# Performance work log

Measured on AMD Instinct MI355X. Metric: run time of the kernel, lower is better.

The kernel has to match this reference:

```python
import jax, jax.numpy as jnp
import numpy as np

D = 128       # embed_dim
UD = 128      # user_embed_dim
NU, NI, NR = 100000, 50000, 10
B, H, S = 4096, 50, 32
EPS = 1e-5


def setup_inputs() -> dict:
    key = jax.random.key(0)
    ks = jax.random.split(key, 24)
    p = lambda k, s: (jax.random.normal(k, s, jnp.float32) * 0.05)
    inp = {
        'u2e': p(ks[0], (NU, D)), 'v2e': p(ks[1], (NI, D)), 'r2e': p(ks[2], (NR, D)),
        'gv_w1': p(ks[3], (2 * D, D)), 'gv_b1': jnp.zeros(D),
        'gv_w2': p(ks[4], (D, D)), 'gv_b2': jnp.zeros(D),
        'atth_w1': p(ks[5], (2 * D, D)), 'atth_b1': jnp.zeros(D),
        'atth_w2': p(ks[6], (D, 1)), 'atth_b2': jnp.zeros(1),
        'enc_w': p(ks[7], (2 * D, D)), 'enc_b': jnp.zeros(D),
        'atts_w1': p(ks[8], (2 * D, D)), 'atts_b1': jnp.zeros(D),
        'atts_w2': p(ks[9], (D, 1)), 'atts_b2': jnp.zeros(1),
        'soc_w': p(ks[10], (2 * D, D)), 'soc_b': jnp.zeros(D),
        'attn_wa': p(ks[11], (D, D)), 'attn_ba': p(ks[12], (D,)),
        'fc1_w': p(ks[13], (D, D)), 'fc1_b': jnp.zeros(D),
        'bn1_g': jnp.ones(D), 'bn1_b': jnp.zeros(D),
        'fc2_w': p(ks[14], (D, UD)), 'fc2_b': jnp.zeros(UD),
        'efc1_w': p(ks[15], (2 * UD, D)), 'efc1_b': jnp.zeros(D),
        'bn2_g': jnp.ones(D), 'bn2_b': jnp.zeros(D),
        'efc2_w': p(ks[16], (D, UD)), 'efc2_b': jnp.zeros(UD),
        'user_ids': jax.random.randint(ks[17], (B, 2), 0, NU),
        'hist_items': jax.random.randint(ks[18], (2 * B, H), 0, NI),
        'hist_ratings': jax.random.randint(ks[19], (2 * B, H), 0, NR),
        'soc_neigh': jax.random.randint(ks[20], (2 * B, S), 0, NU),
    }
    return inp


def _forward(u2e, v2e, r2e, gv_w1, gv_b1, gv_w2, gv_b2, atth_w1, atth_b1, atth_w2, atth_b2,
             enc_w, enc_b, atts_w1, atts_b1, atts_w2, atts_b2, soc_w, soc_b, attn_wa, attn_ba,
             fc1_w, fc1_b, bn1_g, bn1_b, fc2_w, fc2_b, efc1_w, efc1_b, bn2_g, bn2_b,
             efc2_w, efc2_b, user_ids, hist_items, hist_ratings, soc_neigh):
    u = u2e[user_ids.reshape(-1)]                                   # [N,D]
    # --- UV_Aggregator: rating-history aggregation with attention ---
    x = jnp.concatenate([v2e[hist_items], r2e[hist_ratings]], -1)   # [N,H,2D]
    x = jax.nn.relu(x @ gv_w1 + gv_b1)
    x = jax.nn.relu(x @ gv_w2 + gv_b2)                              # [N,H,D]
    q = jnp.broadcast_to(u[:, None, :], x.shape)
    e = jax.nn.relu(jnp.concatenate([x, q], -1) @ atth_w1 + atth_b1) @ atth_w2 + atth_b2
    a = jax.nn.softmax(e, axis=1)                                   # [N,H,1]
    agg = jnp.sum(a * x, axis=1)                                    # [N,D]
    # --- UV_Encoder ---
    h_hist = jax.nn.relu(jnp.concatenate([u, agg], -1) @ enc_w + enc_b)
    # --- Social_Aggregator: neighbor aggregation with attention ---
    nf = u2e[soc_neigh]                                             # [N,S,D]
    qn = jnp.broadcast_to(u[:, None, :], nf.shape)
    es = jax.nn.relu(jnp.concatenate([nf, qn], -1) @ atts_w1 + atts_b1) @ atts_w2 + atts_b2
    a_s = jax.nn.softmax(es, axis=1)
    agg_s = jnp.sum(a_s * nf, axis=1)                               # [N,D]
    # --- Social_Encoder ---
    h = jax.nn.relu(jnp.concatenate([h_hist, agg_s], -1) @ soc_w + soc_b)
    hp = h.reshape(-1, 2, D)                                        # [B,2,D] (initiator, respondent)
    # --- SelfAttentionBatch over each pair ---
    ap = jax.nn.softmax(jnp.tanh(hp @ attn_wa) @ attn_ba, axis=1)   # [B,2]
    w = ap[..., None] * hp                                          # [B,2,D]
    # --- social project head: fc1 -> BN (per-pair batch of 2, train mode) -> relu -> fc2 ---
    y = w @ fc1_w + fc1_b                                           # [B,2,D]
    mu = y.mean(axis=1, keepdims=True)
    var = y.var(axis=1, keepdims=True)
    y = (y - mu) * jax.lax.rsqrt(var + EPS) * bn1_g + bn1_b
    y = jax.nn.relu(y) @ fc2_w + fc2_b                              # [B,2,UD]
    ini, res = y[:, 0], y[:, 1]
    # --- esocial head on concatenated pair reps: fc -> BN over batch -> relu -> fc ---
    c = y.reshape(y.shape[0], -1)                                   # [B,2*UD]
    z = c @ efc1_w + efc1_b                                         # [B,D]
    z = (z - z.mean(0)) * jax.lax.rsqrt(z.var(0) + EPS) * bn2_g + bn2_b
    z = jax.nn.relu(z) @ efc2_w + efc2_b                            # [B,UD]
    return z, ini, res


def reference(u2e, v2e, r2e, gv_w1, gv_b1, gv_w2, gv_b2, atth_w1, atth_b1, atth_w2, atth_b2,
              enc_w, enc_b, atts_w1, atts_b1, atts_w2, atts_b2, soc_w, soc_b, attn_wa, attn_ba,
              fc1_w, fc1_b, bn1_g, bn1_b, fc2_w, fc2_b, efc1_w, efc1_b, bn2_g, bn2_b,
              efc2_w, efc2_b, user_ids, hist_items, hist_ratings, soc_neigh):
    return _forward(u2e, v2e, r2e, gv_w1, gv_b1, gv_w2, gv_b2, atth_w1, atth_b1, atth_w2,
                    atth_b2, enc_w, enc_b, atts_w1, atts_b1, atts_w2, atts_b2, soc_w, soc_b,
                    attn_wa, attn_ba, fc1_w, fc1_b, bn1_g, bn1_b, fc2_w, fc2_b, efc1_w,
                    efc1_b, bn2_g, bn2_b, efc2_w, efc2_b, user_ids, hist_items,
                    hist_ratings, soc_neigh)
```

## Files before the change

kernel.cpp:

```cpp
#include <hip/hip_runtime.h>
#include <hip/hip_bf16.h>
#include <math.h>

#define NROWS   8192
#define HLEN    50
#define SLEN    32
#define NPAIR   4096

typedef __attribute__((ext_vector_type(8))) short   short8;
typedef __attribute__((ext_vector_type(8))) __bf16  b8;
typedef __attribute__((ext_vector_type(4))) float   f32x4;
typedef unsigned short us;

#define A_GV_B1    0
#define A_GV_B2    128
#define A_ATTH_B1  256
#define A_ATTH_W2  384
#define A_ENC_W    512
#define A_ENC_B    33280
#define A_ATTS_B1  33408
#define A_ATTS_W2  33536
#define A_SOC_W    33664
#define A_SOC_B    66432
#define A_ATTN_WA  66560
#define A_ATTN_BA  82944
#define A_FC1_W    83072
#define A_FC1_B    99456
#define A_BN1_G    99584
#define A_BN1_B    99712
#define A_FC2_W    99840
#define A_FC2_B    116224
#define A_EFC1_W   116352
#define A_EFC1_B   149120
#define A_BN2_G    149248
#define A_BN2_B    149376
#define A_EFC2_W   149504
#define A_EFC2_B   165888
#define A_TOTAL    166016

#define WS_HR    0u
#define WS_Z     2097152u
#define WS_ST    4194304u
#define WS_WP1   4195328u
#define WS_WP2   4260864u
#define WS_WPA   4293632u
#define WS_WPS   4359168u
#define WS_AR    4424704u
#define WS_UB    4757504u
#define WS_VB    30357504u
#define WS_RB    43157504u
#define WS2_NEED 43160064u

__device__ __forceinline__ float b2f(us u){
  unsigned int x = ((unsigned int)u) << 16; float f;
  __builtin_memcpy(&f, &x, 4); return f;
}
__device__ __forceinline__ us f2b(float f){
  unsigned int x; __builtin_memcpy(&x, &f, 4);
  return (us)((x + 0x7fffu + ((x >> 16) & 1u)) >> 16);
}
__device__ __forceinline__ us f2bc(float f){
  unsigned int x; __builtin_memcpy(&x, &f, 4);
  return (us)((x + 0x8000u) >> 16);
}
__device__ __forceinline__ float relu(float x){ return 0.5f * (x + fabsf(x)); }

__device__ __forceinline__ b8 f8_to_b8(const float* f){
  short8 v;
#pragma unroll
  for (int j = 0; j < 8; ++j) v[j] = (short)f2bc(f[j]);
  return __builtin_bit_cast(b8, v);
}

typedef __attribute__((address_space(3))) unsigned char lds_b;
typedef const __attribute__((address_space(1))) unsigned char glob_b;

__device__ __forceinline__ void gll16(const us* g, us* d){
  __builtin_amdgcn_global_load_lds((glob_b*)g, (lds_b*)d, 16, 0, 0);
}

__device__ __forceinline__ void stage8k(const us* __restrict__ W, us* sB,
                                        int w8, int l, int ks, int p){
  const us* src = W + ((long)ks << 12) + (w8 << 9) + (l << 3);
  us* dst = sB + (p << 12) + (w8 << 9);
  gll16(src, dst);
}

struct Tbl { const void* p[24]; unsigned off[25]; };
__global__ void k_cvt(Tbl tb, us* __restrict__ AR){
  int i = blockIdx.x * 256 + threadIdx.x;
  if (i >= A_TOTAL) return;
  int s = 0;
  while (i >= (int)tb.off[s + 1]) ++s;
  AR[i] = f2b(((const float*)tb.p[s])[i - (int)tb.off[s]]);
}

__global__ void k_pack(const float* __restrict__ W, us* __restrict__ Wp, int ksegs){
  int g = blockIdx.x * 256 + threadIdx.x;
  if (g >= ksegs * 512) return;
  int lane16 = g & 15, quad = (g >> 4) & 3, nt = (g >> 6) & 7, kseg = g >> 9;
#pragma unroll
  for (int j = 0; j < 8; ++j)
    Wp[(long)g * 8 + j] = f2b(W[(kseg * 32 + quad * 8 + j) * 128 + nt * 16 + lane16]);
}

__global__ void k_tab(const float* __restrict__ src, us* __restrict__ dst, int n8){
  int i = blockIdx.x * 256 + threadIdx.x;
  if (i >= n8) return;
  const float* s = src + (long)i * 8;
  short8 v;
#pragma unroll
  for (int j = 0; j < 8; ++j) v[j] = (short)f2b(s[j]);
  *(short8*)(dst + (long)i * 8) = v;
}

template<int TAB>
__global__ __launch_bounds__(512)
void k_fused(const int* __restrict__ items, const int* __restrict__ ratings,
             const void* __restrict__ vt, const void* __restrict__ rt,
             const int* __restrict__ uids, const void* __restrict__ ut,
             const int* __restrict__ soc,
             const us* __restrict__ Wp1, const us* __restrict__ Wp2,
             const us* __restrict__ WpA, const us* __restrict__ WpS,
             const us* __restrict__ AR, us* __restrict__ HR)
{
  const int t = threadIdx.x;
  const int rr = t >> 8, tt = t & 255;
  const int r = blockIdx.x * 2 + rr;
  const int w = tt >> 6;
  const int w8 = t >> 6;
  const int l = t & 63, lane16 = l & 15, quad = l >> 4;
  const int tc = tt & 127, th = tt >> 7;
  const long ubase = (long)uids[r] * 128;

  __shared__ __align__(16) us sX[2][64 * 136];
  __shared__ __align__(16) us sB[2 * 4096];
  __shared__ float esh[2][64], a_sh[2][64], part[2][256], xin[2][256];

  const int arow = w * 16 + lane16;
  const bool av = arow < HLEN;
  const int it_i = av ? items[r * HLEN + arow]   : 0;
  const int rt_i = av ? ratings[r * HLEN + arow] : 0;

  b8 af[8];
#pragma unroll
  for (int ks = 0; ks < 8; ++ks){
    b8 a;
    if constexpr (TAB){
      const us* ap = (ks < 4)
          ? (const us*)vt + (long)it_i * 128 + ks * 32 + quad * 8
          : (const us*)rt + (long)rt_i * 128 + (ks - 4) * 32 + quad * 8;
      a = *(const b8*)ap;
    } else {
      const float* ap = (ks < 4)
          ? (const float*)vt + (long)it_i * 128 + ks * 32 + quad * 8
          : (const float*)rt + (long)rt_i * 128 + (ks - 4) * 32 + quad * 8;
      a = f8_to_b8(ap);
    }
    if (!av) a = __builtin_bit_cast(b8, (short8)0);
    af[ks] = a;
  }
  b8 uf[4];
#pragma unroll
  for (int ks = 0; ks < 4; ++ks){
    if constexpr (TAB)
      uf[ks] = *(const b8*)((const us*)ut + ubase + ks * 32 + quad * 8);
    else
      uf[ks] = f8_to_b8((const float*)ut + ubase + ks * 32 + quad * 8);
  }

  {
    f32x4 acc[8];
#pragma unroll
    for (int nt = 0; nt < 8; ++nt) acc[nt] = (f32x4){0.f,0.f,0.f,0.f};
    stage8k(Wp1, sB, w8, l, 0, 0);
#pragma unroll
    for (int ks = 0; ks < 8; ++ks){
      __syncthreads();
      if (ks < 7) stage8k(Wp1, sB, w8, l, ks + 1, (ks + 1) & 1);
      const us* bb = sB + ((ks & 1) << 12) + l * 8;
#pragma unroll
      for (int nt = 0; nt < 8; ++nt)
        acc[nt] = __builtin_amdgcn_mfma_f32_16x16x32_bf16(
            af[ks], *(const b8*)(bb + nt * 512), acc[nt], 0, 0, 0);
    }
#pragma unroll
    for (int nt = 0; nt < 8; ++nt){
      int col = nt * 16 + lane16;
      float bbv = b2f(AR[A_GV_B1 + col]);
#pragma unroll
      for (int rg = 0; rg < 4; ++rg)
        sX[rr][(w * 16 + quad * 4 + rg) * 136 + col] = f2bc(relu(acc[nt][rg] + bbv));
    }
  }

  {
    b8 a2[4];
#pragma unroll
    for (int ks = 0; ks < 4; ++ks)
      a2[ks] = *(const b8*)(sX[rr] + arow * 136 + ks * 32 + quad * 8);
    f32x4 acc[8];
#pragma unroll
    for (int nt = 0; nt < 8; ++nt) acc[nt] = (f32x4){0.f,0.f,0.f,0.f};
    stage8k(Wp2, sB, w8, l, 0, 0);
#pragma unroll
    for (int ks = 0; ks < 4; ++ks){
      __syncthreads();
      if (ks < 3) stage8k(Wp2, sB, w8, l, ks + 1, (ks + 1) & 1);
      const us* bb = sB + ((ks & 1) << 12) + l * 8;
#pragma unroll
      for (int nt = 0; nt < 8; ++nt)
        acc[nt] = __builtin_amdgcn_mfma_f32_16x16x32_bf16(
            a2[ks], *(const b8*)(bb + nt * 512), acc[nt], 0, 0, 0);
    }
#pragma unroll
    for (int nt = 0; nt < 8; ++nt){
      int col = nt * 16 + lane16;
      float bbv = b2f(AR[A_GV_B2 + col]);
#pragma unroll
      for (int rg = 0; rg < 4; ++rg)
        sX[rr][(w * 16 + quad * 4 + rg) * 136 + col] = f2bc(relu(acc[nt][rg] + bbv));
    }
  }

  {
    b8 a3[8];
#pragma unroll
    for (int ks = 0; ks < 4; ++ks)
      a3[ks] = *(const b8*)(sX[rr] + arow * 136 + ks * 32 + quad * 8);
#pragma unroll
    for (int ks = 0; ks < 4; ++ks) a3[4 + ks] = uf[ks];
    f32x4 acc[8];
#pragma unroll
    for (int nt = 0; nt < 8; ++nt) acc[nt] = (f32x4){0.f,0.f,0.f,0.f};
    stage8k(WpA, sB, w8, l, 0, 0);
#pragma unroll
    for (int ks = 0; ks < 8; ++ks){
      __syncthreads();
      if (ks < 7) stage8k(WpA, sB, w8, l, ks + 1, (ks + 1) & 1);
      const us* bb = sB + ((ks & 1) << 12) + l * 8;
#pragma unroll
      for (int nt = 0; nt < 8; ++nt)
        acc[nt] = __builtin_amdgcn_mfma_f32_16x16x32_bf16(
            a3[ks], *(const b8*)(bb + nt * 512), acc[nt], 0, 0, 0);
    }
    float pr[4] = {0.f, 0.f, 0.f, 0.f};
#pragma unroll
    for (int nt = 0; nt < 8; ++nt){
      int col = nt * 16 + lane16;
      float bbv = b2f(AR[A_ATTH_B1 + col]);
      float wwv = b2f(AR[A_ATTH_W2 + col]);
#pragma unroll
      for (int rg = 0; rg < 4; ++rg)
        pr[rg] += relu(acc[nt][rg] + bbv) * wwv;
    }
#pragma unroll
    for (int rg = 0; rg < 4; ++rg){
      float p = pr[rg];
      p += __shfl_xor(p, 1, 64);
      p += __shfl_xor(p, 2, 64);
      p += __shfl_xor(p, 4, 64);
      p += __shfl_xor(p, 8, 64);
      if (lane16 == 0) esh[rr][w * 16 + quad * 4 + rg] = p;
    }
  }
  __syncthreads();

  if (tt < 64){
    float e = (tt < HLEN) ? esh[rr][tt] : -1e30f;
    float mx = e;
#pragma unroll
    for (int m = 1; m < 64; m <<= 1) mx = fmaxf(mx, __shfl_xor(mx, m, 64));
    float ex = (tt < HLEN) ? expf(e - mx) : 0.f;
    float s = ex;
#pragma unroll
    for (int m = 1; m < 64; m <<= 1) s += __shfl_xor(s, m, 64);
    if (tt < HLEN) a_sh[rr][tt] = ex / s;
  }
  __syncthreads();

  {
    float s = 0.f;
    for (int h = th * 25; h < th * 25 + 25; ++h)
      s += a_sh[rr][h] * b2f(sX[rr][h * 136 + tc]);
    part[rr][tt] = s;
  }
  __syncthreads();
  if (tt < 128){
    xin[rr][tt] = TAB ? b2f(((const us*)ut)[ubase + tt]) : ((const float*)ut)[ubase + tt];
    xin[rr][128 + tt] = part[rr][tt] + part[rr][128 + tt];
  }
  __syncthreads();

  {
    float s0 = 0.f, s1 = 0.f;
    const int kb = th * 128;
    for (int k = 0; k < 128; k += 2){
      s0 += xin[rr][kb + k]     * b2f(AR[A_ENC_W + (kb + k)     * 128 + tc]);
      s1 += xin[rr][kb + k + 1] * b2f(AR[A_ENC_W + (kb + k + 1) * 128 + tc]);
    }
    part[rr][tt] = s0 + s1;
#pragma unroll
    for (int it = 0; it < 2; ++it){
      int idx = tt * 8 + it * 2048;
      int row = idx >> 7, col = idx & 127;
      long eb = (long)soc[r * SLEN + row] * 128 + col;
      short8 v;
      if constexpr (TAB) v = *(const short8*)((const us*)ut + eb);
      else               v = __builtin_bit_cast(short8, f8_to_b8((const float*)ut + eb));
      *(short8*)(sX[rr] + row * 136 + col) = v;
    }
  }
  stage8k(WpS, sB, w8, l, 0, 0);
  __syncthreads();

  float hhv = 0.f;
  if (tt < 128)
    hhv = relu(part[rr][tt] + part[rr][128 + tt] + b2f(AR[A_ENC_B + tt]));

  {
    const int mt = w & 1, nh = w >> 1;
    const int arow2 = mt * 16 + lane16;
    b8 aS[8];
#pragma unroll
    for (int ks = 0; ks < 4; ++ks)
      aS[ks] = *(const b8*)(sX[rr] + arow2 * 136 + ks * 32 + quad * 8);
#pragma unroll
    for (int ks = 0; ks < 4; ++ks) aS[4 + ks] = uf[ks];
    f32x4 acc[4];
#pragma unroll
    for (int nt = 0; nt < 4; ++nt) acc[nt] = (f32x4){0.f,0.f,0.f,0.f};
#pragma unroll
    for (int ks = 0; ks < 8; ++ks){
      __syncthreads();
      if (ks < 7) stage8k(WpS, sB, w8, l, ks + 1, (ks + 1) & 1);
      const us* bb = sB + ((ks & 1) << 12) + (nh << 11) + l * 8;
#pragma unroll
      for (int nt = 0; nt < 4; ++nt)
        acc[nt] = __builtin_amdgcn_mfma_f32_16x16x32_bf16(
            aS[ks], *(const b8*)(bb + nt * 512), acc[nt], 0, 0, 0);
    }
    float pr[4] = {0.f, 0.f, 0.f, 0.f};
#pragma unroll
    for (int nt = 0; nt < 4; ++nt){
      int n = nh * 64 + nt * 16 + lane16;
      float bbv = b2f(AR[A_ATTS_B1 + n]);
      float wwv = b2f(AR[A_ATTS_W2 + n]);
#pragma unroll
      for (int rg = 0; rg < 4; ++rg)
        pr[rg] += relu(acc[nt][rg] + bbv) * wwv;
    }
#pragma unroll
    for (int rg = 0; rg < 4; ++rg){
      float p = pr[rg];
      p += __shfl_xor(p, 1, 64);
      p += __shfl_xor(p, 2, 64);
      p += __shfl_xor(p, 4, 64);
      p += __shfl_xor(p, 8, 64);
      if (lane16 == 0) esh[rr][nh * 32 + mt * 16 + quad * 4 + rg] = p;
    }
  }
  __syncthreads();

  if (tt < 32){
    float e = esh[rr][tt] + esh[rr][32 + tt];
    float mx = e;
#pragma unroll
    for (int m = 1; m < 32; m <<= 1) mx = fmaxf(mx, __shfl_xor(mx, m, 32));
    float ex = expf(e - mx);
    float s = ex;
#pragma unroll
    for (int m = 1; m < 32; m <<= 1) s += __shfl_xor(s, m, 32);
    a_sh[rr][tt] = ex / s;
  }
  __syncthreads();

  {
    float s = 0.f;
    for (int h = th * 16; h < th * 16 + 16; ++h)
      s += a_sh[rr][h] * b2f(sX[rr][h * 136 + tc]);
    part[rr][tt] = s;
  }
  __syncthreads();
  if (tt < 128){
    xin[rr][tt]       = hhv;
    xin[rr][128 + tt] = part[rr][tt] + part[rr][128 + tt];
  }
  __syncthreads();

  {
    float s0 = 0.f, s1 = 0.f;
    const int kb = th * 128;
    for (int k = 0; k < 128; k += 2){
      s0 += xin[rr][kb + k]     * b2f(AR[A_SOC_W + (kb + k)     * 128 + tc]);
      s1 += xin[rr][kb + k + 1] * b2f(AR[A_SOC_W + (kb + k + 1) * 128 + tc]);
    }
    part[rr][tt] = s0 + s1;
  }
  __syncthreads();
  if (tt < 128)
    HR[(long)r * 128 + tt] =
        f2bc(relu(part[rr][tt] + part[rr][128 + tt] + b2f(AR[A_SOC_B + tt])));
}

__global__ void k7_head(const us* __restrict__ HR, const us* __restrict__ AR,
                        float* __restrict__ OUT, float* __restrict__ Z)
{
  const int i = blockIdx.x, t = threadIdx.x;
  const int j = t >> 7, d = t & 127;
  __shared__ float hp[2][128], ysh[2][128], ry[2][128], csh[256], p2[2][128];
  __shared__ float sred[4];

  hp[j][d] = b2f(HR[(long)(2 * i + j) * 128 + d]);
  __syncthreads();

  float v0 = 0.f, v1 = 0.f;
  for (int k = 0; k < 128; k += 2){
    v0 += hp[j][k]     * b2f(AR[A_ATTN_WA + k * 128 + d]);
    v1 += hp[j][k + 1] * b2f(AR[A_ATTN_WA + (k + 1) * 128 + d]);
  }
  float part = tanhf(v0 + v1) * b2f(AR[A_ATTN_BA + d]);
#pragma unroll
  for (int m = 1; m < 64; m <<= 1) part += __shfl_xor(part, m, 64);
  if ((t & 63) == 0) sred[t >> 6] = part;
  __syncthreads();

  float s0 = sred[0] + sred[1], s1 = sred[2] + sred[3];
  float mx = fmaxf(s0, s1);
  float e0 = expf(s0 - mx), e1 = expf(s1 - mx);
  float aj = (j ? e1 : e0) / (e0 + e1);

  v0 = 0.f; v1 = 0.f;
  for (int k = 0; k < 128; k += 2){
    v0 += hp[j][k]     * b2f(AR[A_FC1_W + k * 128 + d]);
    v1 += hp[j][k + 1] * b2f(AR[A_FC1_W + (k + 1) * 128 + d]);
  }
  ysh[j][d] = aj * (v0 + v1) + b2f(AR[A_FC1_B + d]);
  __syncthreads();

  if (t < 128){
    float y0 = ysh[0][t], y1 = ysh[1][t];
    float mu = 0.5f * (y0 + y1);
    float dv = 0.5f * (y0 - y1);
    float rs = rsqrtf(dv * dv + 1e-5f);
    float g = b2f(AR[A_BN1_G + t]), bb = b2f(AR[A_BN1_B + t]);
    ry[0][t] = relu((y0 - mu) * rs * g + bb);
    ry[1][t] = relu((y1 - mu) * rs * g + bb);
  }
  __syncthreads();

  v0 = 0.f; v1 = 0.f;
  for (int k = 0; k < 128; k += 2){
    v0 += ry[j][k]     * b2f(AR[A_FC2_W + k * 128 + d]);
    v1 += ry[j][k + 1] * b2f(AR[A_FC2_W + (k + 1) * 128 + d]);
  }
  float y2 = v0 + v1 + b2f(AR[A_FC2_B + d]);
  OUT[(long)(j ? 2 * NPAIR * 128 : NPAIR * 128) + (long)i * 128 + d] = y2;
  csh[j * 128 + d] = y2;
  __syncthreads();

  {
    const int kh = t >> 7, d2 = t & 127;
    v0 = 0.f; v1 = 0.f;
    for (int k = 0; k < 128; k += 2){
      v0 += csh[kh * 128 + k]     * b2f(AR[A_EFC1_W + (kh * 128 + k) * 128 + d2]);
      v1 += csh[kh * 128 + k + 1] * b2f(AR[A_EFC1_W + (kh * 128 + k + 1) * 128 + d2]);
    }
    p2[kh][d2] = v0 + v1;
  }
  __syncthreads();
  if (t < 128)
    Z[(long)i * 128 + t] = p2[0][t] + p2[1][t] + b2f(AR[A_EFC1_B + t]);
}

__global__ void k8_stats(const float* __restrict__ Z, float* __restrict__ ST){
  const int c = blockIdx.x, t = threadIdx.x;
  float s = 0.f, s2 = 0.f;
  for (int row = t; row < NPAIR; row += 256){
    float v = Z[(long)row * 128 + c];
    s += v; s2 += v * v;
  }
#pragma unroll
  for (int m = 1; m < 64; m <<= 1){ s += __shfl_xor(s, m, 64); s2 += __shfl_xor(s2, m, 64); }
  __shared__ float red[8];
  if ((t & 63) == 0){ red[t >> 6] = s; red[4 + (t >> 6)] = s2; }
  __syncthreads();
  if (t == 0){
    float S  = red[0] + red[1] + red[2] + red[3];
    float S2 = red[4] + red[5] + red[6] + red[7];
    float mean = S / (float)NPAIR;
    float var  = S2 / (float)NPAIR - mean * mean;
    ST[c]       = mean;
    ST[128 + c] = rsqrtf(var + 1e-5f);
  }
}

__global__ void k9_final(const float* __restrict__ Z, const float* __restrict__ ST,
                         const us* __restrict__ AR, float* __restrict__ OUT)
{
  const int i = blockIdx.x, t = threadIdx.x;
  __shared__ float zn[128];
  float zv = Z[(long)i * 128 + t];
  zn[t] = relu((zv - ST[t]) * ST[128 + t] * b2f(AR[A_BN2_G + t]) + b2f(AR[A_BN2_B + t]));
  __syncthreads();
  float v0 = 0.f, v1 = 0.f;
  for (int k = 0; k < 128; k += 2){
    v0 += zn[k]     * b2f(AR[A_EFC2_W + k * 128 + t]);
    v1 += zn[k + 1] * b2f(AR[A_EFC2_W + (k + 1) * 128 + t]);
  }
  OUT[(long)i * 128 + t] = v0 + v1 + b2f(AR[A_EFC2_B + t]);
}

extern "C" void kernel_launch(void* const* d_in, const int* in_sizes, int n_in,
                              void* d_out, int out_size, void* d_ws, size_t ws_size,
                              hipStream_t stream)
{
  const float* u2e = (const float*)d_in[0];
  const float* v2e = (const float*)d_in[1];
  const float* r2e = (const float*)d_in[2];
  const int* user_ids     = (const int*)d_in[33];
  const int* hist_items   = (const int*)d_in[34];
  const int* hist_ratings = (const int*)d_in[35];
  const int* soc_neigh    = (const int*)d_in[36];

  char* ws = (char*)d_ws;
  us*    HR  = (us*)(ws + WS_HR);
  float* Z   = (float*)(ws + WS_Z);
  float* ST  = (float*)(ws + WS_ST);
  us*    Wp1 = (us*)(ws + WS_WP1);
  us*    Wp2 = (us*)(ws + WS_WP2);
  us*    WpA = (us*)(ws + WS_WPA);
  us*    WpS = (us*)(ws + WS_WPS);
  us*    AR  = (us*)(ws + WS_AR);
  us*    Ub  = (us*)(ws + WS_UB);
  us*    Vb  = (us*)(ws + WS_VB);
  us*    Rb  = (us*)(ws + WS_RB);
  float* OUT = (float*)d_out;

  const bool big = ws_size >= (size_t)WS2_NEED;

  Tbl tb;
  const void* sp[24] = {d_in[4], d_in[6], d_in[8], d_in[9], d_in[11], d_in[12],
                        d_in[14], d_in[15], d_in[17], d_in[18], d_in[19], d_in[20],
                        d_in[21], d_in[22], d_in[23], d_in[24], d_in[25], d_in[26],
                        d_in[27], d_in[28], d_in[29], d_in[30], d_in[31], d_in[32]};
  const unsigned offs[25] = {0,128,256,384,512,33280,33408,33536,33664,66432,
                             66560,82944,83072,99456,99584,99712,99840,116224,
                             116352,149120,149248,149376,149504,165888,166016};
  for (int i = 0; i < 24; ++i) tb.p[i] = sp[i];
  for (int i = 0; i < 25; ++i) tb.off[i] = offs[i];
  k_cvt<<<(A_TOTAL + 255) / 256, 256, 0, stream>>>(tb, AR);

  k_pack<<<16, 256, 0, stream>>>((const float*)d_in[3],  Wp1, 8);
  k_pack<<< 8, 256, 0, stream>>>((const float*)d_in[5],  Wp2, 4);
  k_pack<<<16, 256, 0, stream>>>((const float*)d_in[7],  WpA, 8);
  k_pack<<<16, 256, 0, stream>>>((const float*)d_in[13], WpS, 8);

  if (big){
    k_tab<<<(1600000 + 255) / 256, 256, 0, stream>>>(u2e, Ub, 1600000);
    k_tab<<<( 800000 + 255) / 256, 256, 0, stream>>>(v2e, Vb,  800000);
    k_tab<<<(    160 + 255) / 256, 256, 0, stream>>>(r2e, Rb,     160);
    k_fused<1><<<NROWS / 2, 512, 0, stream>>>(hist_items, hist_ratings, Vb, Rb,
        user_ids, Ub, soc_neigh, Wp1, Wp2, WpA, WpS, AR, HR);
  } else {
    k_fused<0><<<NROWS / 2, 512, 0, stream>>>(hist_items, hist_ratings, v2e, r2e,
        user_ids, u2e, soc_neigh, Wp1, Wp2, WpA, WpS, AR, HR);
  }

  k7_head<<<NPAIR, 256, 0, stream>>>(HR, AR, OUT, Z);
  k8_stats<<<128, 256, 0, stream>>>(Z, ST);
  k9_final<<<NPAIR, 128, 0, stream>>>(Z, ST, AR, OUT);
}
```

Before: 499.3 us.

## Transpose dense weights for vectorized row reads and use lighter phase barriers

Adds a pre-pass that stores the dense-layer weights (enc, soc, attn, fc1, fc2, efc1, efc2) as transposed bf16, so each thread reads its output column's weights contiguously with 16-byte vector loads. Before, each thread did strided scalar 2-byte loads. It also replaces __syncthreads in the MFMA staging loops with an explicit vmcnt(0) wait plus s_barrier and a sched_barrier. The cost is seven extra small conversion launches and more workspace. Each thread now reads from a different row, which may reduce coalescing across lanes.

```diff
diff --git a/kernel.cpp b/kernel.cpp
--- a/kernel.cpp
+++ b/kernel.cpp
@@ -38,6 +38,15 @@
 #define A_EFC2_B   165888
 #define A_TOTAL    166016
 
+#define T_ENC_W    0
+#define T_SOC_W    32768
+#define T_ATTN_WA  65536
+#define T_FC1_W    81920
+#define T_FC2_W    98304
+#define T_EFC1_W   114688
+#define T_EFC2_W   147456
+#define T_TOTAL    163840
+
 #define WS_HR    0u
 #define WS_Z     2097152u
 #define WS_ST    4194304u
@@ -46,10 +55,11 @@
 #define WS_WPA   4293632u
 #define WS_WPS   4359168u
 #define WS_AR    4424704u
-#define WS_UB    4757504u
-#define WS_VB    30357504u
-#define WS_RB    43157504u
-#define WS2_NEED 43160064u
+#define WS_ART   4756736u
+#define WS_UB    5084416u
+#define WS_VB    30684416u
+#define WS_RB    43484416u
+#define WS2_NEED 43486976u
 
 __device__ __forceinline__ float b2f(us u){
   unsigned int x = ((unsigned int)u) << 16; float f;
@@ -85,6 +95,13 @@
   us* dst = sB + (p << 12) + (w8 << 9);
   gll16(src, dst);
 }
+
+#define PHASE_SYNC() do {                                   \
+    asm volatile("s_waitcnt vmcnt(0)" ::: "memory");        \
+    __builtin_amdgcn_s_barrier();                           \
+    asm volatile("" ::: "memory");                          \
+    __builtin_amdgcn_sched_barrier(0);                      \
+  } while (0)
 
 struct Tbl { const void* p[24]; unsigned off[25]; };
 __global__ void k_cvt(Tbl tb, us* __restrict__ AR){
@@ -93,6 +110,13 @@
   int s = 0;
   while (i >= (int)tb.off[s + 1]) ++s;
   AR[i] = f2b(((const float*)tb.p[s])[i - (int)tb.off[s]]);
+}
+
+__global__ void k_cvtT(const float* __restrict__ src, us* __restrict__ dst, int K){
+  int g = blockIdx.x * 256 + threadIdx.x;
+  if (g >= K * 128) return;
+  int k = g >> 7, n = g & 127;
+  dst[n * K + k] = f2b(src[g]);
 }
 
 __global__ void k_pack(const float* __restrict__ W, us* __restrict__ Wp, int ksegs){
@@ -122,7 +146,8 @@
              const int* __restrict__ soc,
              const us* __restrict__ Wp1, const us* __restrict__ Wp2,
              const us* __restrict__ WpA, const us* __restrict__ WpS,
-             const us* __restrict__ AR, us* __restrict__ HR)
+             const us* __restrict__ AR, const us* __restrict__ ART,
+             us* __restrict__ HR)
 {
   const int t = threadIdx.x;
   const int rr = t >> 8, tt = t & 255;
@@ -176,7 +201,7 @@
     stage8k(Wp1, sB, w8, l, 0, 0);
 #pragma unroll
     for (int ks = 0; ks < 8; ++ks){
-      __syncthreads();
+      PHASE_SYNC();
       if (ks < 7) stage8k(Wp1, sB, w8, l, ks + 1, (ks + 1) & 1);
       const us* bb = sB + ((ks & 1) << 12) + l * 8;
 #pragma unroll
@@ -205,7 +230,7 @@
     stage8k(Wp2, sB, w8, l, 0, 0);
 #pragma unroll
     for (int ks = 0; ks < 4; ++ks){
-      __syncthreads();
+      PHASE_SYNC();
       if (ks < 3) stage8k(Wp2, sB, w8, l, ks + 1, (ks + 1) & 1);
       const us* bb = sB + ((ks & 1) << 12) + l * 8;
 #pragma unroll
@@ -236,7 +261,7 @@
     stage8k(WpA, sB, w8, l, 0, 0);
 #pragma unroll
     for (int ks = 0; ks < 8; ++ks){
-      __syncthreads();
+      PHASE_SYNC();
       if (ks < 7) stage8k(WpA, sB, w8, l, ks + 1, (ks + 1) & 1);
       const us* bb = sB + ((ks & 1) << 12) + l * 8;
 #pragma unroll
@@ -295,9 +320,16 @@
   {
     float s0 = 0.f, s1 = 0.f;
     const int kb = th * 128;
-    for (int k = 0; k < 128; k += 2){
-      s0 += xin[rr][kb + k]     * b2f(AR[A_ENC_W + (kb + k)     * 128 + tc]);
-      s1 += xin[rr][kb + k + 1] * b2f(AR[A_ENC_W + (kb + k + 1) * 128 + tc]);
+    const us* wt = ART + T_ENC_W + (long)tc * 256 + kb;
+    const float* xp = &xin[rr][kb];
+#pragma unroll
+    for (int k8 = 0; k8 < 128; k8 += 8){
+      short8 wv = *(const short8*)(wt + k8);
+#pragma unroll
+      for (int jj = 0; jj < 8; jj += 2){
+        s0 += xp[k8 + jj]     * b2f((us)wv[jj]);
+        s1 += xp[k8 + jj + 1] * b2f((us)wv[jj + 1]);
+      }
     }
     part[rr][tt] = s0 + s1;
 #pragma unroll
@@ -332,7 +364,7 @@
     for (int nt = 0; nt < 4; ++nt) acc[nt] = (f32x4){0.f,0.f,0.f,0.f};
 #pragma unroll
     for (int ks = 0; ks < 8; ++ks){
-      __syncthreads();
+      PHASE_SYNC();
       if (ks < 7) stage8k(WpS, sB, w8, l, ks + 1, (ks + 1) & 1);
       const us* bb = sB + ((ks & 1) << 12) + (nh << 11) + l * 8;
 #pragma unroll
@@ -391,9 +423,16 @@
   {
     float s0 = 0.f, s1 = 0.f;
     const int kb = th * 128;
-    for (int k = 0; k < 128; k += 2){
-      s0 += xin[rr][kb + k]     * b2f(AR[A_SOC_W + (kb + k)     * 128 + tc]);
-      s1 += xin[rr][kb + k + 1] * b2f(AR[A_SOC_W + (kb + k + 1) * 128 + tc]);
+    const us* wt = ART + T_SOC_W + (long)tc * 256 + kb;
+    const float* xp = &xin[rr][kb];
+#pragma unroll
+    for (int k8 = 0; k8 < 128; k8 += 8){
+      short8 wv = *(const short8*)(wt + k8);
+#pragma unroll
+      for (int jj = 0; jj < 8; jj += 2){
+        s0 += xp[k8 + jj]     * b2f((us)wv[jj]);
+        s1 += xp[k8 + jj + 1] * b2f((us)wv[jj + 1]);
+      }
     }
     part[rr][tt] = s0 + s1;
   }
@@ -404,6 +443,7 @@
 }
 
 __global__ void k7_head(const us* __restrict__ HR, const us* __restrict__ AR,
+                        const us* __restrict__ ART,
                         float* __restrict__ OUT, float* __restrict__ Z)
 {
   const int i = blockIdx.x, t = threadIdx.x;
@@ -415,9 +455,17 @@
   __syncthreads();
 
   float v0 = 0.f, v1 = 0.f;
-  for (int k = 0; k < 128; k += 2){
-    v0 += hp[j][k]     * b2f(AR[A_ATTN_WA + k * 128 + d]);
-    v1 += hp[j][k + 1] * b2f(AR[A_ATTN_WA + (k + 1) * 128 + d]);
+  {
+    const us* wt = ART + T_ATTN_WA + (long)d * 128;
+#pragma unroll
+    for (int k8 = 0; k8 < 128; k8 += 8){
+      short8 wv = *(const short8*)(wt + k8);
+#pragma unroll
+      for (int jj = 0; jj < 8; jj += 2){
+        v0 += hp[j][k8 + jj]     * b2f((us)wv[jj]);
+        v1 += hp[j][k8 + jj + 1] * b2f((us)wv[jj + 1]);
+      }
+    }
   }
   float part = tanhf(v0 + v1) * b2f(AR[A_ATTN_BA + d]);
 #pragma unroll
@@ -431,9 +479,17 @@
   float aj = (j ? e1 : e0) / (e0 + e1);
 
   v0 = 0.f; v1 = 0.f;
-  for (int k = 0; k < 128; k += 2){
-    v0 += hp[j][k]     * b2f(AR[A_FC1_W + k * 128 + d]);
-    v1 += hp[j][k + 1] * b2f(AR[A_FC1_W + (k + 1) * 128 + d]);
+  {
+    const us* wt = ART + T_FC1_W + (long)d * 128;
+#pragma unroll
+    for (int k8 = 0; k8 < 128; k8 += 8){
+      short8 wv = *(const short8*)(wt + k8);
+#pragma unroll
+      for (int jj = 0; jj < 8; jj += 2){
+        v0 += hp[j][k8 + jj]     * b2f((us)wv[jj]);
+        v1 += hp[j][k8 + jj + 1] * b2f((us)wv[jj + 1]);
+      }
+    }
   }
   ysh[j][d] = aj * (v0 + v1) + b2f(AR[A_FC1_B + d]);
   __syncthreads();
@@ -450,9 +506,17 @@
   __syncthreads();
 
   v0 = 0.f; v1 = 0.f;
-  for (int k = 0; k < 128; k += 2){
-    v0 += ry[j][k]     * b2f(AR[A_FC2_W + k * 128 + d]);
-    v1 += ry[j][k + 1] * b2f(AR[A_FC2_W + (k + 1) * 128 + d]);
+  {
+    const us* wt = ART + T_FC2_W + (long)d * 128;
+#pragma unroll
+    for (int k8 = 0; k8 < 128; k8 += 8){
+      short8 wv = *(const short8*)(wt + k8);
+#pragma unroll
+      for (int jj = 0; jj < 8; jj += 2){
+        v0 += ry[j][k8 + jj]     * b2f((us)wv[jj]);
+        v1 += ry[j][k8 + jj + 1] * b2f((us)wv[jj + 1]);
+      }
+    }
   }
   float y2 = v0 + v1 + b2f(AR[A_FC2_B + d]);
   OUT[(long)(j ? 2 * NPAIR * 128 : NPAIR * 128) + (long)i * 128 + d] = y2;
@@ -461,10 +525,17 @@
 
   {
     const int kh = t >> 7, d2 = t & 127;
+    const us* wt = ART + T_EFC1_W + (long)d2 * 256 + kh * 128;
+    const float* cp = &csh[kh * 128];
     v0 = 0.f; v1 = 0.f;
-    for (int k = 0; k < 128; k += 2){
-      v0 += csh[kh * 128 + k]     * b2f(AR[A_EFC1_W + (kh * 128 + k) * 128 + d2]);
-      v1 += csh[kh * 128 + k + 1] * b2f(AR[A_EFC1_W + (kh * 128 + k + 1) * 128 + d2]);
+#pragma unroll
+    for (int k8 = 0; k8 < 128; k8 += 8){
+      short8 wv = *(const short8*)(wt + k8);
+#pragma unroll
+      for (int jj = 0; jj < 8; jj += 2){
+        v0 += cp[k8 + jj]     * b2f((us)wv[jj]);
+        v1 += cp[k8 + jj + 1] * b2f((us)wv[jj + 1]);
+      }
     }
     p2[kh][d2] = v0 + v1;
   }
@@ -496,7 +567,8 @@
 }
 
 __global__ void k9_final(const float* __restrict__ Z, const float* __restrict__ ST,
-                         const us* __restrict__ AR, float* __restrict__ OUT)
+                         const us* __restrict__ AR, const us* __restrict__ ART,
+                         float* __restrict__ OUT)
 {
   const int i = blockIdx.x, t = threadIdx.x;
   __shared__ float zn[128];
@@ -504,9 +576,17 @@
   zn[t] = relu((zv - ST[t]) * ST[128 + t] * b2f(AR[A_BN2_G + t]) + b2f(AR[A_BN2_B + t]));
   __syncthreads();
   float v0 = 0.f, v1 = 0.f;
-  for (int k = 0; k < 128; k += 2){
-    v0 += zn[k]     * b2f(AR[A_EFC2_W + k * 128 + t]);
-    v1 += zn[k + 1] * b2f(AR[A_EFC2_W + (k + 1) * 128 + t]);
+  {
+    const us* wt = ART + T_EFC2_W + (long)t * 128;
+#pragma unroll
+    for (int k8 = 0; k8 < 128; k8 += 8){
+      short8 wv = *(const short8*)(wt + k8);
+#pragma unroll
+      for (int jj = 0; jj < 8; jj += 2){
+        v0 += zn[k8 + jj]     * b2f((us)wv[jj]);
+        v1 += zn[k8 + jj + 1] * b2f((us)wv[jj + 1]);
+      }
+    }
   }
   OUT[(long)i * 128 + t] = v0 + v1 + b2f(AR[A_EFC2_B + t]);
 }
@@ -532,6 +612,7 @@
   us*    WpA = (us*)(ws + WS_WPA);
   us*    WpS = (us*)(ws + WS_WPS);
   us*    AR  = (us*)(ws + WS_AR);
+  us*    ART = (us*)(ws + WS_ART);
   us*    Ub  = (us*)(ws + WS_UB);
   us*    Vb  = (us*)(ws + WS_VB);
   us*    Rb  = (us*)(ws + WS_RB);
@@ -556,18 +637,26 @@
   k_pack<<<16, 256, 0, stream>>>((const float*)d_in[7],  WpA, 8);
   k_pack<<<16, 256, 0, stream>>>((const float*)d_in[13], WpS, 8);
 
+  k_cvtT<<<128, 256, 0, stream>>>((const float*)d_in[11], ART + T_ENC_W,   256);
+  k_cvtT<<<128, 256, 0, stream>>>((const float*)d_in[17], ART + T_SOC_W,   256);
+  k_cvtT<<< 64, 256, 0, stream>>>((const float*)d_in[19], ART + T_ATTN_WA, 128);
+  k_cvtT<<< 64, 256, 0, stream>>>((const float*)d_in[21], ART + T_FC1_W,   128);
+  k_cvtT<<< 64, 256, 0, stream>>>((const float*)d_in[25], ART + T_FC2_W,   128);
+  k_cvtT<<<128, 256, 0, stream>>>((const float*)d_in[27], ART + T_EFC1_W,  256);
+  k_cvtT<<< 64, 256, 0, stream>>>((const float*)d_in[31], ART + T_EFC2_W,  128);
+
   if (big){
     k_tab<<<(1600000 + 255) / 256, 256, 0, stream>>>(u2e, Ub, 1600000);
     k_tab<<<( 800000 + 255) / 256, 256, 0, stream>>>(v2e, Vb,  800000);
     k_tab<<<(    160 + 255) / 256, 256, 0, stream>>>(r2e, Rb,     160);
     k_fused<1><<<NROWS / 2, 512, 0, stream>>>(hist_items, hist_ratings, Vb, Rb,
-        user_ids, Ub, soc_neigh, Wp1, Wp2, WpA, WpS, AR, HR);
+        user_ids, Ub, soc_neigh, Wp1, Wp2, WpA, WpS, AR, ART, HR);
   } else {
     k_fused<0><<<NROWS / 2, 512, 0, stream>>>(hist_items, hist_ratings, v2e, r2e,
-        user_ids, u2e, soc_neigh, Wp1, Wp2, WpA, WpS, AR, HR);
-  }
-
-  k7_head<<<NPAIR, 256, 0, stream>>>(HR, AR, OUT, Z);
+        user_ids, u2e, soc_neigh, Wp1, Wp2, WpA, WpS, AR, ART, HR);
+  }
+
+  k7_head<<<NPAIR, 256, 0, stream>>>(HR, AR, ART, OUT, Z);
   k8_stats<<<128, 256, 0, stream>>>(Z, ST);
-  k9_final<<<NPAIR, 128, 0, stream>>>(Z, ST, AR, OUT);
-}
+  k9_final<<<NPAIR, 128, 0, stream>>>(Z, ST, AR, ART, OUT);
+}
```

Result: slower. 753.3 us (+50.9%).
